# Optimization experiments

Measured on AMD Instinct MI355X. Metric: run time of the kernel, lower is better.

## Reference

```python
import jax, jax.numpy as jnp
import numpy as np
from jax import lax

B, T, E = 64, 1024, 512
H, NSTACK = 512, 2


def setup_inputs() -> dict:
    key = jax.random.key(0)
    ks = jax.random.split(key, 7)
    seq = jax.random.normal(ks[0], (B, T, E), dtype=jnp.float32)
    seq_len = jax.random.randint(ks[1], (B,), 1, T + 1)
    seq_len = seq_len.at[0].set(T)  # torch sizes output by max(seq_len); pin it to T
    s = 1.0 / np.sqrt(H)
    W_ih = jax.random.uniform(ks[2], (NSTACK, 4 * H, E), jnp.float32, -s, s)
    W_hh = jax.random.uniform(ks[3], (NSTACK, 4 * H, H), jnp.float32, -s, s)
    b_ih = jax.random.uniform(ks[4], (NSTACK, 4 * H), jnp.float32, -s, s)
    b_hh = jax.random.uniform(ks[5], (NSTACK, 4 * H), jnp.float32, -s, s)
    return {"seq": seq, "seq_len": seq_len, "W_ih": W_ih, "W_hh": W_hh,
            "b_ih": b_ih, "b_hh": b_hh}


def _encoder_step(x, h, c, W_ih, W_hh, b_ih, b_hh):
    """One time step of the nStack residual LSTM. x:[B,E], h/c:[nStack,B,H]."""
    nh, nc = [], []
    inp = x
    for s in range(W_ih.shape[0]):
        gates = inp @ W_ih[s].T + h[s] @ W_hh[s].T + b_ih[s] + b_hh[s]
        i, f, g, o = jnp.split(gates, 4, axis=-1)
        i, f, o = jax.nn.sigmoid(i), jax.nn.sigmoid(f), jax.nn.sigmoid(o)
        g = jnp.tanh(g)
        cs = f * c[s] + i * g
        hs = o * jnp.tanh(cs)
        inp = hs + inp  # residual (E == H)
        nh.append(hs)
        nc.append(cs)
    return inp, jnp.stack(nh), jnp.stack(nc)


def reference(seq, seq_len, W_ih, W_hh, b_ih, b_hh):
    # Masked full-batch recurrence == torch's sorted shrinking-batch loop:
    # inactive rows (t >= seq_len) keep their state and write 0 hiddens.
    b, t, _ = seq.shape
    nstack = W_ih.shape[0]
    hidden = W_hh.shape[-1]
    h0 = jnp.zeros((nstack, b, hidden), seq.dtype)
    c0 = jnp.zeros((nstack, b, hidden), seq.dtype)
    mask_t = jnp.arange(t)[:, None] < seq_len[None, :]  # [T,B]

    def step(carry, xt):
        h, c = carry
        x, m = xt  # x:[B,E], m:[B]
        hx, nh, nc = _encoder_step(x, h, c, W_ih, W_hh, b_ih, b_hh)
        mm = m[None, :, None]
        h = jnp.where(mm, nh, h)
        c = jnp.where(mm, nc, c)
        out = jnp.where(m[:, None], hx, jnp.zeros_like(hx))
        return (h, c), out

    (h, c), outs = lax.scan(step, (h0, c0), (jnp.swapaxes(seq, 0, 1), mask_t))
    total_hiddens = jnp.swapaxes(outs, 0, 1)  # [B,T,H]
    return total_hiddens, h, c
```

## Files before the change

kernel.cpp:

```cpp
#include <hip/hip_runtime.h>
#include <stdint.h>

#define BB 64
#define TT 1024
#define HH 512
typedef unsigned long long ull;
typedef float v4f __attribute__((ext_vector_type(4)));
typedef short v8s __attribute__((ext_vector_type(8)));
typedef unsigned v4u __attribute__((ext_vector_type(4)));

__device__ __forceinline__ short f2bf(float f) {
    unsigned u = __float_as_uint(f);
    u += 0x7fffu + ((u >> 16) & 1u);
    return (short)(u >> 16);
}
__device__ __forceinline__ float sigmoidf_(float x) {
    x = fminf(fmaxf(x, -30.f), 30.f);
    return 1.f / (1.f + __expf(-x));
}
__device__ __forceinline__ float tanhf_(float x) {
    x = fminf(fmaxf(x, -15.f), 15.f);
    float e = __expf(2.f * x);
    return (e - 1.f) / (e + 1.f);
}

__device__ __forceinline__ unsigned aload32(const unsigned* p) {
    return __hip_atomic_load(p, __ATOMIC_RELAXED, __HIP_MEMORY_SCOPE_AGENT);
}
__device__ __forceinline__ void wait_ge(unsigned* c, unsigned tgt) {
    while (__hip_atomic_load(c, __ATOMIC_RELAXED, __HIP_MEMORY_SCOPE_AGENT) < tgt)
        __builtin_amdgcn_s_sleep(1);
}
__device__ __forceinline__ void stcc(unsigned* p, unsigned v) {
    asm volatile("global_store_dword %0, %1, off sc0 sc1" :: "v"(p), "v"(v) : "memory");
}
__device__ __forceinline__ void ld4cc(const unsigned* p, v4u& r0, v4u& r1, v4u& r2, v4u& r3) {
    asm volatile(
        "global_load_dwordx4 %0, %4, off sc0 sc1\n\t"
        "global_load_dwordx4 %1, %4, off offset:16 sc0 sc1\n\t"
        "global_load_dwordx4 %2, %4, off offset:2048 sc0 sc1\n\t"
        "global_load_dwordx4 %3, %4, off offset:2064 sc0 sc1\n\t"
        "s_waitcnt vmcnt(0)"
        : "=&v"(r0), "=&v"(r1), "=&v"(r2), "=&v"(r3)
        : "v"(p) : "memory");
}
__device__ __forceinline__ void ld8cc(const unsigned* px, const unsigned* ph,
        v4u& x0, v4u& x1, v4u& x2, v4u& x3, v4u& h0, v4u& h1, v4u& h2, v4u& h3) {
    asm volatile(
        "global_load_dwordx4 %0, %8, off sc0 sc1\n\t"
        "global_load_dwordx4 %1, %8, off offset:16 sc0 sc1\n\t"
        "global_load_dwordx4 %2, %8, off offset:2048 sc0 sc1\n\t"
        "global_load_dwordx4 %3, %8, off offset:2064 sc0 sc1\n\t"
        "global_load_dwordx4 %4, %9, off sc0 sc1\n\t"
        "global_load_dwordx4 %5, %9, off offset:16 sc0 sc1\n\t"
        "global_load_dwordx4 %6, %9, off offset:2048 sc0 sc1\n\t"
        "global_load_dwordx4 %7, %9, off offset:2064 sc0 sc1\n\t"
        "s_waitcnt vmcnt(0)"
        : "=&v"(x0), "=&v"(x1), "=&v"(x2), "=&v"(x3),
          "=&v"(h0), "=&v"(h1), "=&v"(h2), "=&v"(h3)
        : "v"(px), "v"(ph) : "memory");
}
__device__ __forceinline__ unsigned tagdiff(v4u a, v4u b, unsigned tg) {
    return ((a.x ^ tg) | (a.y ^ tg) | (a.z ^ tg) | (a.w ^ tg) |
            (b.x ^ tg) | (b.y ^ tg) | (b.z ^ tg) | (b.w ^ tg)) & 0xFFFFu;
}
__device__ __forceinline__ void packlds(short* dst, v4u a, v4u b) {
    v4u d;
    d.x = (a.x >> 16) | (a.y & 0xFFFF0000u);
    d.y = (a.z >> 16) | (a.w & 0xFFFF0000u);
    d.z = (b.x >> 16) | (b.y & 0xFFFF0000u);
    d.w = (b.z >> 16) | (b.w & 0xFFFF0000u);
    *(v4u*)dst = d;
}

__global__ __launch_bounds__(512, 1) void lstm_persistent_kernel(
    const float* __restrict__ seq, const int* __restrict__ seq_len,
    const float* __restrict__ W_ih, const float* __restrict__ W_hh,
    const float* __restrict__ b_ih, const float* __restrict__ b_hh,
    float* __restrict__ out, char* __restrict__ ws)
{
    __shared__ __align__(16) short act_lds[2048 * 8];
    __shared__ float gates_lds[4][16][32];

    const int gid = blockIdx.x;
    const int g   = gid & 3;
    const int s   = (gid >> 2) & 1;
    const int u0  = (gid >> 3) << 5;
    const int bg  = g << 4;
    const int tid = threadIdx.x;
    const int w   = tid >> 6;
    const int l   = tid & 63;
    const int q   = w >> 1;
    const int uh  = w & 1;
    const int quad = l >> 4, l15 = l & 15;
    const int cb  = tid >> 5, cu = tid & 31;

    unsigned* rc1 = (unsigned*)(ws + g * 256);
    unsigned* h0b = (unsigned*)(ws + 1024);
    unsigned* h1b = h0b + 4 * 4 * 16 * 512;
    unsigned* ibb = h1b + 4 * 4 * 16 * 512;

    const float* Wi = W_ih + (size_t)s * (2048 * 512);
    const float* Wh = W_hh + (size_t)s * (2048 * 512);
    const int row = q * 512 + u0 + uh * 16 + l15;
    v8s wf[32];
#pragma unroll
    for (int kt = 0; kt < 32; ++kt) {
        int ko = kt * 32 + quad * 8;
        const float* p = (ko < 512) ? (Wi + (size_t)row * 512 + ko)
                                    : (Wh + (size_t)row * 512 + (ko - 512));
        float4 x0 = *(const float4*)p;
        float4 x1 = *(const float4*)(p + 4);
        v8s v;
        v[0]=f2bf(x0.x); v[1]=f2bf(x0.y); v[2]=f2bf(x0.z); v[3]=f2bf(x0.w);
        v[4]=f2bf(x1.x); v[5]=f2bf(x1.y); v[6]=f2bf(x1.z); v[7]=f2bf(x1.w);
        wf[kt] = v;
    }
    float bias[4];
#pragma unroll
    for (int qq = 0; qq < 4; ++qq)
        bias[qq] = b_ih[s * 2048 + qq * 512 + u0 + cu] + b_hh[s * 2048 + qq * 512 + u0 + cu];
    const int len = seq_len[bg + cb];
    float hreg = 0.f, creg = 0.f;

    const int ch0 = 1024 + (tid << 1);
    const int mh  = ch0 & 15;
    const int kh  = (((ch0 >> 6) << 5) + (((ch0 >> 4) & 3) << 3)) - 512;
    const int cx0 = tid << 1;
    const int mx  = cx0 & 15;
    const int kx  = ((cx0 >> 6) << 5) + (((cx0 >> 4) & 3) << 3);
    unsigned* myhb = (s == 0) ? h0b : h1b;

    for (int tau = 0; tau <= TT; ++tau) {
        if (s == 0 && tau >= TT) break;
        if (s == 1 && tau == 0) continue;
        const int t   = (s == 0) ? tau : tau - 1;
        const int rb  = (((tau - 1) & 3) << 2 | g) << 13;
        const int wb  = ((tau & 3) << 2 | g) << 13;
        const unsigned tg = (unsigned)(tau - 1);
        float xres = 0.f;
        unsigned rcv = 0xFFFFFFFFu;

        if (s == 0) {
            if (tid == 0 && tau >= 4) rcv = aload32(rc1);
#pragma unroll
            for (int j = 0; j < 2; ++j) {
                int c = (j << 9) + tid;
                int ll = c & 63, m = ll & 15;
                int ko = ((c >> 6) << 5) + ((ll >> 4) << 3);
                const float* p = seq + (((size_t)(bg + m) * TT + t) << 9) + ko;
                float4 x0 = *(const float4*)p, x1 = *(const float4*)(p + 4);
                v8s v;
                v[0]=f2bf(x0.x); v[1]=f2bf(x0.y); v[2]=f2bf(x0.z); v[3]=f2bf(x0.w);
                v[4]=f2bf(x1.x); v[5]=f2bf(x1.y); v[6]=f2bf(x1.z); v[7]=f2bf(x1.w);
                *(v8s*)(act_lds + (size_t)c * 8) = v;
            }
            xres = seq[(((size_t)(bg + cb) * TT + t) << 9) + u0 + cu];
            if (tau == 0) {
                v4u zz = {0, 0, 0, 0};
                *(v4u*)(act_lds + (size_t)ch0 * 8) = zz;
                *(v4u*)(act_lds + (size_t)(ch0 + 1) * 8) = zz;
            } else {
                const unsigned* hp = h0b + rb + (mh << 9) + kh;
                for (;;) {
                    v4u r0, r1, r2, r3;
                    ld4cc(hp, r0, r1, r2, r3);
                    if ((tagdiff(r0, r1, tg) | tagdiff(r2, r3, tg)) == 0) {
                        packlds(act_lds + (size_t)ch0 * 8, r0, r1);
                        packlds(act_lds + (size_t)(ch0 + 1) * 8, r2, r3);
                        break;
                    }
                }
            }
        } else {
            const unsigned* px = ibb + rb + (mx << 9) + kx;
            if (tau == 1) {
                v4u zz = {0, 0, 0, 0};
                *(v4u*)(act_lds + (size_t)ch0 * 8) = zz;
                *(v4u*)(act_lds + (size_t)(ch0 + 1) * 8) = zz;
                for (;;) {
                    v4u r0, r1, r2, r3;
                    ld4cc(px, r0, r1, r2, r3);
                    if ((tagdiff(r0, r1, tg) | tagdiff(r2, r3, tg)) == 0) {
                        packlds(act_lds + (size_t)cx0 * 8, r0, r1);
                        packlds(act_lds + (size_t)(cx0 + 1) * 8, r2, r3);
                        break;
                    }
                }
            } else {
                const unsigned* ph = h1b + rb + (mh << 9) + kh;
                for (;;) {
                    v4u x0, x1, x2, x3, h0, h1, h2, h3;
                    ld8cc(px, ph, x0, x1, x2, x3, h0, h1, h2, h3);
                    if ((tagdiff(x0, x1, tg) | tagdiff(x2, x3, tg) |
                         tagdiff(h0, h1, tg) | tagdiff(h2, h3, tg)) == 0) {
                        packlds(act_lds + (size_t)cx0 * 8, x0, x1);
                        packlds(act_lds + (size_t)(cx0 + 1) * 8, x2, x3);
                        packlds(act_lds + (size_t)ch0 * 8, h0, h1);
                        packlds(act_lds + (size_t)(ch0 + 1) * 8, h2, h3);
                        break;
                    }
                }
            }
        }
        __syncthreads();
        if (s == 1 && tid == 0)
            __hip_atomic_fetch_add(rc1, 1u, __ATOMIC_RELAXED, __HIP_MEMORY_SCOPE_AGENT);

        v4f z = {0.f, 0.f, 0.f, 0.f};
        v4f acc0 = z, acc1 = z, acc2 = z, acc3 = z;
#pragma unroll
        for (int kt = 0; kt < 32; kt += 4) {
            v8s a0 = *(const v8s*)(act_lds + ((kt + 0) * 64 + l) * 8);
            v8s a1 = *(const v8s*)(act_lds + ((kt + 1) * 64 + l) * 8);
            v8s a2 = *(const v8s*)(act_lds + ((kt + 2) * 64 + l) * 8);
            v8s a3 = *(const v8s*)(act_lds + ((kt + 3) * 64 + l) * 8);
            acc0 = __builtin_amdgcn_mfma_f32_16x16x32_bf16(a0, wf[kt + 0], acc0, 0, 0, 0);
            acc1 = __builtin_amdgcn_mfma_f32_16x16x32_bf16(a1, wf[kt + 1], acc1, 0, 0, 0);
            acc2 = __builtin_amdgcn_mfma_f32_16x16x32_bf16(a2, wf[kt + 2], acc2, 0, 0, 0);
            acc3 = __builtin_amdgcn_mfma_f32_16x16x32_bf16(a3, wf[kt + 3], acc3, 0, 0, 0);
        }
        v4f af = (acc0 + acc1) + (acc2 + acc3);
#pragma unroll
        for (int r = 0; r < 4; ++r)
            gates_lds[q][quad * 4 + r][uh * 16 + l15] = af[r];
        __syncthreads();

        float gi = gates_lds[0][cb][cu] + bias[0];
        float gf = gates_lds[1][cb][cu] + bias[1];
        float gg = gates_lds[2][cb][cu] + bias[2];
        float go = gates_lds[3][cb][cu] + bias[3];
        float ii = sigmoidf_(gi), ff = sigmoidf_(gf);
        float gv = tanhf_(gg),   oo = sigmoidf_(go);
        float cs = ff * creg + ii * gv;
        float hs = oo * tanhf_(cs);
        const bool msk = (t < len);
        if (msk) { creg = cs; hreg = hs; }

        const unsigned otg = (unsigned)tau;
        const int widx = wb + (cb << 9) + u0 + cu;
        stcc(myhb + widx, (((unsigned)(unsigned short)f2bf(hreg)) << 16) | otg);

        float i1s = 0.f;
        if (s == 0) {
            i1s = hs + xres;
        } else {
            int k  = u0 + cu;
            int cI = ((k >> 5) << 6) + (((k >> 3) & 3) << 4) + cb;
            unsigned short us = (unsigned short)act_lds[cI * 8 + (k & 7)];
            float i1 = __uint_as_float(((unsigned)us) << 16);
            out[(((size_t)(bg + cb) * TT + t) << 9) + u0 + cu] = msk ? (i1 + hs) : 0.f;
        }
        if (s == 0 && tid == 0 && tau >= 4) {
            unsigned need = 16u * (unsigned)(tau - 3);
            if (rcv < need) wait_ge(rc1, need);
        }
        __syncthreads();

        if (s == 0)
            stcc(ibb + widx, (((unsigned)(unsigned short)f2bf(i1s)) << 16) | otg);
    }

    const size_t OH = (size_t)BB * TT * HH;
    const size_t hoff = OH + (size_t)s * BB * HH + ((size_t)(bg + cb) << 9) + u0 + cu;
    out[hoff] = hreg;
    out[hoff + (size_t)2 * BB * HH] = creg;
}

extern "C" void kernel_launch(void* const* d_in, const int* in_sizes, int n_in,
                              void* d_out, int out_size, void* d_ws, size_t ws_size,
                              hipStream_t stream) {
    const float* seq     = (const float*)d_in[0];
    const int*   seq_len = (const int*)d_in[1];
    const float* W_ih    = (const float*)d_in[2];
    const float* W_hh    = (const float*)d_in[3];
    const float* b_ih    = (const float*)d_in[4];
    const float* b_hh    = (const float*)d_in[5];
    float* out = (float*)d_out;

    hipMemsetAsync(d_ws, 0, 1024, stream);

    lstm_persistent_kernel<<<dim3(128), dim3(512), 0, stream>>>(
        seq, seq_len, W_ih, W_hh, b_ih, b_hh, out, (char*)d_ws);
}
```

Before: 4.025 ms.

## Overlap recurrent h polling with input-half MFMAs in persistent LSTM

Splits each step's K loop into an input half and a recurrent half. The recurrent-state poll load is issued early and the input-half MFMAs run while it is in flight; the h values are then tag-checked, packed into LDS, and the second half runs after another barrier. This hides cross-block h latency on the critical path. In exchange it adds a second barrier per step, moves the rc1 credit increment until after the gate barrier (which may delay producers), and keeps a fallback spin loop for when the tags are not yet ready.

Result: slower. 4.226 ms (+5.0%).

```diff
diff --git a/kernel.cpp b/kernel.cpp
--- a/kernel.cpp
+++ b/kernel.cpp
@@ -44,21 +44,18 @@
         : "=&v"(r0), "=&v"(r1), "=&v"(r2), "=&v"(r3)
         : "v"(p) : "memory");
 }
-__device__ __forceinline__ void ld8cc(const unsigned* px, const unsigned* ph,
-        v4u& x0, v4u& x1, v4u& x2, v4u& x3, v4u& h0, v4u& h1, v4u& h2, v4u& h3) {
+__device__ __forceinline__ void ld4cc_issue(const unsigned* p, v4u& r0, v4u& r1, v4u& r2, v4u& r3) {
     asm volatile(
-        "global_load_dwordx4 %0, %8, off sc0 sc1\n\t"
-        "global_load_dwordx4 %1, %8, off offset:16 sc0 sc1\n\t"
-        "global_load_dwordx4 %2, %8, off offset:2048 sc0 sc1\n\t"
-        "global_load_dwordx4 %3, %8, off offset:2064 sc0 sc1\n\t"
-        "global_load_dwordx4 %4, %9, off sc0 sc1\n\t"
-        "global_load_dwordx4 %5, %9, off offset:16 sc0 sc1\n\t"
-        "global_load_dwordx4 %6, %9, off offset:2048 sc0 sc1\n\t"
-        "global_load_dwordx4 %7, %9, off offset:2064 sc0 sc1\n\t"
-        "s_waitcnt vmcnt(0)"
-        : "=&v"(x0), "=&v"(x1), "=&v"(x2), "=&v"(x3),
-          "=&v"(h0), "=&v"(h1), "=&v"(h2), "=&v"(h3)
-        : "v"(px), "v"(ph) : "memory");
+        "global_load_dwordx4 %0, %4, off sc0 sc1\n\t"
+        "global_load_dwordx4 %1, %4, off offset:16 sc0 sc1\n\t"
+        "global_load_dwordx4 %2, %4, off offset:2048 sc0 sc1\n\t"
+        "global_load_dwordx4 %3, %4, off offset:2064 sc0 sc1"
+        : "=&v"(r0), "=&v"(r1), "=&v"(r2), "=&v"(r3)
+        : "v"(p) : "memory");
+}
+__device__ __forceinline__ void vmwait4(v4u& r0, v4u& r1, v4u& r2, v4u& r3) {
+    asm volatile("s_waitcnt vmcnt(0)"
+        : "+v"(r0), "+v"(r1), "+v"(r2), "+v"(r3) :: "memory");
 }
 __device__ __forceinline__ unsigned tagdiff(v4u a, v4u b, unsigned tg) {
     return ((a.x ^ tg) | (a.y ^ tg) | (a.z ^ tg) | (a.w ^ tg) |
@@ -72,6 +69,24 @@
     d.w = (b.z >> 16) | (b.w & 0xFFFF0000u);
     *(v4u*)dst = d;
 }
+__device__ __forceinline__ void lds_barrier() {
+    asm volatile("s_waitcnt lgkmcnt(0)" ::: "memory");
+    __builtin_amdgcn_s_barrier();
+    __builtin_amdgcn_sched_barrier(0);
+}
+
+#define MFMA_HALF(KT0)                                                        \
+    _Pragma("unroll")                                                         \
+    for (int kt = (KT0); kt < (KT0) + 16; kt += 4) {                          \
+        v8s a0 = *(const v8s*)(act_lds + ((kt + 0) * 64 + l) * 8);            \
+        v8s a1 = *(const v8s*)(act_lds + ((kt + 1) * 64 + l) * 8);            \
+        v8s a2 = *(const v8s*)(act_lds + ((kt + 2) * 64 + l) * 8);            \
+        v8s a3 = *(const v8s*)(act_lds + ((kt + 3) * 64 + l) * 8);            \
+        acc0 = __builtin_amdgcn_mfma_f32_16x16x32_bf16(a0, wf[kt + 0], acc0, 0, 0, 0); \
+        acc1 = __builtin_amdgcn_mfma_f32_16x16x32_bf16(a1, wf[kt + 1], acc1, 0, 0, 0); \
+        acc2 = __builtin_amdgcn_mfma_f32_16x16x32_bf16(a2, wf[kt + 2], acc2, 0, 0, 0); \
+        acc3 = __builtin_amdgcn_mfma_f32_16x16x32_bf16(a3, wf[kt + 3], acc3, 0, 0, 0); \
+    }
 
 __global__ __launch_bounds__(512, 1) void lstm_persistent_kernel(
     const float* __restrict__ seq, const int* __restrict__ seq_len,
@@ -141,7 +156,15 @@
         float xres = 0.f;
         unsigned rcv = 0xFFFFFFFFu;
 
+        v4f z = {0.f, 0.f, 0.f, 0.f};
+        v4f acc0 = z, acc1 = z, acc2 = z, acc3 = z;
+        v4u p0, p1, p2, p3;
+        const unsigned* hp;
+        bool hpoll;
+
         if (s == 0) {
+            hp = h0b + rb + (mh << 9) + kh;
+            hpoll = (tau >= 1);
             if (tid == 0 && tau >= 4) rcv = aload32(rc1);
 #pragma unroll
             for (int j = 0; j < 2; ++j) {
@@ -156,12 +179,43 @@
                 *(v8s*)(act_lds + (size_t)c * 8) = v;
             }
             xres = seq[(((size_t)(bg + cb) * TT + t) << 9) + u0 + cu];
-            if (tau == 0) {
+            if (hpoll) {
+                ld4cc_issue(hp, p0, p1, p2, p3);
+            } else {
                 v4u zz = {0, 0, 0, 0};
                 *(v4u*)(act_lds + (size_t)ch0 * 8) = zz;
                 *(v4u*)(act_lds + (size_t)(ch0 + 1) * 8) = zz;
+            }
+        } else {
+            hp = h1b + rb + (mh << 9) + kh;
+            hpoll = (tau >= 2);
+            const unsigned* px = ibb + rb + (mx << 9) + kx;
+            if (tau == 1) {
+                v4u zz = {0, 0, 0, 0};
+                *(v4u*)(act_lds + (size_t)ch0 * 8) = zz;
+                *(v4u*)(act_lds + (size_t)(ch0 + 1) * 8) = zz;
+            }
+            for (;;) {
+                v4u r0, r1, r2, r3;
+                ld4cc(px, r0, r1, r2, r3);
+                if ((tagdiff(r0, r1, tg) | tagdiff(r2, r3, tg)) == 0) {
+                    packlds(act_lds + (size_t)cx0 * 8, r0, r1);
+                    packlds(act_lds + (size_t)(cx0 + 1) * 8, r2, r3);
+                    break;
+                }
+            }
+            if (hpoll) ld4cc_issue(hp, p0, p1, p2, p3);
+        }
+
+        lds_barrier();
+        MFMA_HALF(0)
+
+        if (hpoll) {
+            vmwait4(p0, p1, p2, p3);
+            if ((tagdiff(p0, p1, tg) | tagdiff(p2, p3, tg)) == 0) {
+                packlds(act_lds + (size_t)ch0 * 8, p0, p1);
+                packlds(act_lds + (size_t)(ch0 + 1) * 8, p2, p3);
             } else {
-                const unsigned* hp = h0b + rb + (mh << 9) + kh;
                 for (;;) {
                     v4u r0, r1, r2, r3;
                     ld4cc(hp, r0, r1, r2, r3);
@@ -172,59 +226,18 @@
                     }
                 }
             }
-        } else {
-            const unsigned* px = ibb + rb + (mx << 9) + kx;
-            if (tau == 1) {
-                v4u zz = {0, 0, 0, 0};
-                *(v4u*)(act_lds + (size_t)ch0 * 8) = zz;
-                *(v4u*)(act_lds + (size_t)(ch0 + 1) * 8) = zz;
-                for (;;) {
-                    v4u r0, r1, r2, r3;
-                    ld4cc(px, r0, r1, r2, r3);
-                    if ((tagdiff(r0, r1, tg) | tagdiff(r2, r3, tg)) == 0) {
-                        packlds(act_lds + (size_t)cx0 * 8, r0, r1);
-                        packlds(act_lds + (size_t)(cx0 + 1) * 8, r2, r3);
-                        break;
-                    }
-                }
-            } else {
-                const unsigned* ph = h1b + rb + (mh << 9) + kh;
-                for (;;) {
-                    v4u x0, x1, x2, x3, h0, h1, h2, h3;
-                    ld8cc(px, ph, x0, x1, x2, x3, h0, h1, h2, h3);
-                    if ((tagdiff(x0, x1, tg) | tagdiff(x2, x3, tg) |
-                         tagdiff(h0, h1, tg) | tagdiff(h2, h3, tg)) == 0) {
-                        packlds(act_lds + (size_t)cx0 * 8, x0, x1);
-                        packlds(act_lds + (size_t)(cx0 + 1) * 8, x2, x3);
-                        packlds(act_lds + (size_t)ch0 * 8, h0, h1);
-                        packlds(act_lds + (size_t)(ch0 + 1) * 8, h2, h3);
-                        break;
-                    }
-                }
-            }
-        }
-        __syncthreads();
-        if (s == 1 && tid == 0)
-            __hip_atomic_fetch_add(rc1, 1u, __ATOMIC_RELAXED, __HIP_MEMORY_SCOPE_AGENT);
-
-        v4f z = {0.f, 0.f, 0.f, 0.f};
-        v4f acc0 = z, acc1 = z, acc2 = z, acc3 = z;
-#pragma unroll
-        for (int kt = 0; kt < 32; kt += 4) {
-            v8s a0 = *(const v8s*)(act_lds + ((kt + 0) * 64 + l) * 8);
-            v8s a1 = *(const v8s*)(act_lds + ((kt + 1) * 64 + l) * 8);
-            v8s a2 = *(const v8s*)(act_lds + ((kt + 2) * 64 + l) * 8);
-            v8s a3 = *(const v8s*)(act_lds + ((kt + 3) * 64 + l) * 8);
-            acc0 = __builtin_amdgcn_mfma_f32_16x16x32_bf16(a0, wf[kt + 0], acc0, 0, 0, 0);
-            acc1 = __builtin_amdgcn_mfma_f32_16x16x32_bf16(a1, wf[kt + 1], acc1, 0, 0, 0);
-            acc2 = __builtin_amdgcn_mfma_f32_16x16x32_bf16(a2, wf[kt + 2], acc2, 0, 0, 0);
-            acc3 = __builtin_amdgcn_mfma_f32_16x16x32_bf16(a3, wf[kt + 3], acc3, 0, 0, 0);
-        }
+            lds_barrier();
+        }
+        MFMA_HALF(16)
+
         v4f af = (acc0 + acc1) + (acc2 + acc3);
 #pragma unroll
         for (int r = 0; r < 4; ++r)
             gates_lds[q][quad * 4 + r][uh * 16 + l15] = af[r];
         __syncthreads();
+
+        if (s == 1 && tid == 0)
+            __hip_atomic_fetch_add(rc1, 1u, __ATOMIC_RELAXED, __HIP_MEMORY_SCOPE_AGENT);
 
         float gi = gates_lds[0][cb][cu] + bias[0];
         float gf = gates_lds[1][cb][cu] + bias[1];
```
